# Kernel optimization log

Hardware: AMD Instinct MI355X
Metric: run time of the kernel (lower is better)

## Reference

```python
import jax, jax.numpy as jnp
import numpy as np

N_NODES, N_EDGES, DIM, N_GRAPHS = 200000, 400000, 256, 2048


def _mlp_params(key, dim):
    # MLP([dim, dim//2, dim//4, 1]) -> 3 Linear layers
    k1, k2, k3 = jax.random.split(key, 3)
    def lin(k, fi, fo):
        s = 1.0 / np.sqrt(fi)
        kw, kb = jax.random.split(k)
        W = jax.random.uniform(kw, (fi, fo), jnp.float32, -s, s)
        b = jax.random.uniform(kb, (fo,), jnp.float32, -s, s)
        return W, b
    W1, b1 = lin(k1, dim, dim // 2)
    W2, b2 = lin(k2, dim // 2, dim // 4)
    W3, b3 = lin(k3, dim // 4, 1)
    return W1, b1, W2, b2, W3, b3


def setup_inputs() -> dict:
    key = jax.random.key(0)
    kn, ke, kin, kie, kpn, kpe = jax.random.split(key, 6)
    emb_nodes = jax.random.normal(kn, (N_NODES, DIM), jnp.float32)
    emb_edges = jax.random.normal(ke, (N_EDGES, DIM), jnp.float32)
    node_index = jnp.sort(jax.random.randint(kin, (N_NODES,), 0, N_GRAPHS, jnp.int32))
    edge_index = jnp.sort(jax.random.randint(kie, (N_EDGES,), 0, N_GRAPHS, jnp.int32))
    Wn1, bn1, Wn2, bn2, Wn3, bn3 = _mlp_params(kpn, DIM)
    We1, be1, We2, be2, We3, be3 = _mlp_params(kpe, DIM)
    return {
        "emb_nodes": emb_nodes, "emb_edges": emb_edges,
        "node_index": node_index, "edge_index": edge_index,
        "Wn1": Wn1, "bn1": bn1, "Wn2": Wn2, "bn2": bn2, "Wn3": Wn3, "bn3": bn3,
        "We1": We1, "be1": be1, "We2": We2, "be2": be2, "We3": We3, "be3": be3,
        "num_graphs": N_GRAPHS,
    }


def _gated_att_pool(src, index, W1, b1, W2, b2, W3, b3, num_segments):
    # att MLP: dim -> dim/2 -> dim/4 -> 1 (ReLU between hidden layers)
    h = jax.nn.relu(src @ W1 + b1)
    h = jax.nn.relu(h @ W2 + b2)
    logits = (h @ W3 + b3).reshape(-1)  # [N]
    # scatter_softmax over segments (numerically stable)
    m = jax.ops.segment_max(logits, index, num_segments=num_segments)
    e = jnp.exp(logits - m[index])
    s = jax.ops.segment_sum(e, index, num_segments=num_segments)
    att = (e / s[index])[:, None]  # [N,1]
    # weighted scatter_add -> [num_segments, dim]
    return jax.ops.segment_sum(att * src, index, num_segments=num_segments)


def reference(emb_nodes, emb_edges, node_index, edge_index,
              Wn1, bn1, Wn2, bn2, Wn3, bn3,
              We1, be1, We2, be2, We3, be3, num_graphs):
    nodes_pooled = _gated_att_pool(emb_nodes, node_index, Wn1, bn1, Wn2, bn2, Wn3, bn3, num_graphs)
    edges_pooled = _gated_att_pool(emb_edges, edge_index, We1, be1, We2, be2, We3, be3, num_graphs)
    return nodes_pooled, edges_pooled
```

## Files before the change

### kernel.cpp

```cpp
#include <hip/hip_runtime.h>

typedef unsigned short ushort_t;
typedef __attribute__((ext_vector_type(8))) short short8;
typedef __attribute__((ext_vector_type(4))) float f32x4;

__device__ __forceinline__ ushort_t f2bf(float f) {
    union { float f; unsigned int u; } c; c.f = f;
    unsigned int r = c.u + 0x7fffu + ((c.u >> 16) & 1u);
    return (ushort_t)(r >> 16);
}

__global__ __launch_bounds__(256) void build_wfrags(
    const float* __restrict__ W1, const float* __restrict__ W2,
    ushort_t* __restrict__ W1f, ushort_t* __restrict__ W2f)
{
    int tid = blockIdx.x * 256 + threadIdx.x;
    if (tid < 32768) {
        int j = tid & 7, l = (tid >> 3) & 63, fi = tid >> 9;
        int nt = fi >> 3, kt = fi & 7;
        int n = nt * 16 + (l & 15);
        int k = kt * 32 + (l >> 4) * 8 + j;
        W1f[tid] = f2bf(W1[k * 128 + n]);
    } else if (tid < 40960) {
        int u = tid - 32768;
        int j = u & 7, l = (u >> 3) & 63, fi = u >> 9;
        int nt = fi >> 2, kt = fi & 3;
        int n = nt * 16 + (l & 15);
        int k = kt * 32 + (l >> 4) * 8 + j;
        W2f[u] = f2bf(W2[k * 64 + n]);
    }
}

#define MLP_WAVES 8
#define MLP_TPW 1
#define MLP_LDS_BYTES (16384 + MLP_WAVES * 16 * 136 * 2)

__global__ __launch_bounds__(512, 4) void mlp_logits(
    const float* __restrict__ X, const ushort_t* __restrict__ W1f,
    const ushort_t* __restrict__ W2f, const float* __restrict__ b1,
    const float* __restrict__ b2, const float* __restrict__ W3,
    const float* __restrict__ b3, float* __restrict__ logits, int nsub)
{
    extern __shared__ __align__(16) char smem[];
    ushort_t* W2s    = (ushort_t*)smem;
    ushort_t* h1base = (ushort_t*)(smem + 16384);

    const int t = threadIdx.x;
    const int w = t >> 6, lane = t & 63;
    const int q = lane >> 4, c16 = lane & 15;

    {
        const f32x4* s2 = (const f32x4*)W2f; f32x4* d2 = (f32x4*)smem;
        for (int i = t; i < 1024; i += 512) d2[i] = s2[i];
    }
    __syncthreads();

    float bias1[8], bias2[4], w3v[4];
    #pragma unroll
    for (int nt = 0; nt < 8; ++nt) bias1[nt] = b1[nt * 16 + c16];
    #pragma unroll
    for (int nt = 0; nt < 4; ++nt) bias2[nt] = b2[nt * 16 + c16];
    #pragma unroll
    for (int nt = 0; nt < 4; ++nt) w3v[nt] = W3[nt * 16 + c16];
    const float b3v = b3[0];

    ushort_t* hw = h1base + w * (16 * 136);

    for (int sub = 0; sub < MLP_TPW; ++sub) {
        const int s = (blockIdx.x * MLP_WAVES + w) * MLP_TPW + sub;
        if (s >= nsub) break;
        const float* xp = X + (size_t)(s * 16 + c16) * 256 + q * 8;

        short8 av[8];
        {
            f32x4 xv[8];
            #pragma unroll
            for (int kt = 0; kt < 4; ++kt) {
                xv[2 * kt]     = *(const f32x4*)(xp + kt * 32);
                xv[2 * kt + 1] = *(const f32x4*)(xp + kt * 32 + 4);
            }
            #pragma unroll
            for (int kt = 0; kt < 4; ++kt)
                #pragma unroll
                for (int j = 0; j < 4; ++j) {
                    av[kt][j]     = (short)f2bf(xv[2 * kt][j]);
                    av[kt][4 + j] = (short)f2bf(xv[2 * kt + 1][j]);
                }
            #pragma unroll
            for (int kt = 4; kt < 8; ++kt) {
                xv[2 * (kt - 4)]     = *(const f32x4*)(xp + kt * 32);
                xv[2 * (kt - 4) + 1] = *(const f32x4*)(xp + kt * 32 + 4);
            }
            #pragma unroll
            for (int kt = 4; kt < 8; ++kt)
                #pragma unroll
                for (int j = 0; j < 4; ++j) {
                    av[kt][j]     = (short)f2bf(xv[2 * (kt - 4)][j]);
                    av[kt][4 + j] = (short)f2bf(xv[2 * (kt - 4) + 1][j]);
                }
        }

        f32x4 acc[8];
        #pragma unroll
        for (int nt = 0; nt < 8; ++nt) acc[nt] = (f32x4){0.f, 0.f, 0.f, 0.f};
        #pragma unroll
        for (int kt = 0; kt < 8; ++kt) {
            #pragma unroll
            for (int nt = 0; nt < 8; ++nt) {
                short8 bf = *(const short8*)(W1f + ((nt * 8 + kt) * 64 + lane) * 8);
                acc[nt] = __builtin_amdgcn_mfma_f32_16x16x32_bf16(av[kt], bf, acc[nt], 0, 0, 0);
            }
        }

        #pragma unroll
        for (int nt = 0; nt < 8; ++nt)
            #pragma unroll
            for (int reg = 0; reg < 4; ++reg)
                hw[(q * 4 + reg) * 136 + nt * 16 + c16] =
                    f2bf(fmaxf(acc[nt][reg] + bias1[nt], 0.f));

        f32x4 acc2[4];
        #pragma unroll
        for (int nt = 0; nt < 4; ++nt) acc2[nt] = (f32x4){0.f, 0.f, 0.f, 0.f};
        #pragma unroll
        for (int kt = 0; kt < 4; ++kt) {
            short8 a = *(const short8*)(hw + c16 * 136 + kt * 32 + q * 8);
            #pragma unroll
            for (int nt = 0; nt < 4; ++nt) {
                short8 bf = *(const short8*)(W2s + ((nt * 4 + kt) * 64 + lane) * 8);
                acc2[nt] = __builtin_amdgcn_mfma_f32_16x16x32_bf16(a, bf, acc2[nt], 0, 0, 0);
            }
        }

        float p[4];
        #pragma unroll
        for (int reg = 0; reg < 4; ++reg) {
            float v = 0.f;
            #pragma unroll
            for (int nt = 0; nt < 4; ++nt)
                v += fmaxf(acc2[nt][reg] + bias2[nt], 0.f) * w3v[nt];
            p[reg] = v;
        }
        #pragma unroll
        for (int msk = 1; msk < 16; msk <<= 1)
            #pragma unroll
            for (int reg = 0; reg < 4; ++reg)
                p[reg] += __shfl_xor(p[reg], msk);
        if (c16 == 0) {
            #pragma unroll
            for (int reg = 0; reg < 4; ++reg)
                logits[s * 16 + q * 4 + reg] = p[reg] + b3v;
        }
    }
}

__global__ __launch_bounds__(256) void pool(
    const float* __restrict__ X, const int* __restrict__ idx,
    const float* __restrict__ logits, float* __restrict__ out, int nrows)
{
    const int g = blockIdx.x;
    const int t = threadIdx.x;
    const int w = t >> 6, lane = t & 63;

    int lo = 0, hi = nrows;
    while (lo < hi) { int mid = (lo + hi) >> 1; if (idx[mid] < g) lo = mid + 1; else hi = mid; }
    const int start = lo;
    hi = nrows;
    while (lo < hi) { int mid = (lo + hi) >> 1; if (idx[mid] < g + 1) lo = mid + 1; else hi = mid; }
    const int cnt = lo - start;

    __shared__ float red[8];
    __shared__ float parts[4][256];

    const float* lg = logits + start;

    float m = -3.0e38f;
    for (int i = t; i < cnt; i += 256) m = fmaxf(m, lg[i]);
    #pragma unroll
    for (int o = 32; o; o >>= 1) m = fmaxf(m, __shfl_xor(m, o));
    if (lane == 0) red[w] = m;
    __syncthreads();
    m = fmaxf(fmaxf(red[0], red[1]), fmaxf(red[2], red[3]));

    float ssum = 0.f;
    for (int i = t; i < cnt; i += 256) ssum += __expf(lg[i] - m);
    #pragma unroll
    for (int o = 32; o; o >>= 1) ssum += __shfl_xor(ssum, o);
    if (lane == 0) red[4 + w] = ssum;
    __syncthreads();
    ssum = red[4] + red[5] + red[6] + red[7];
    const float inv = (cnt > 0) ? 1.f / ssum : 0.f;

    f32x4 acc = {0.f, 0.f, 0.f, 0.f};
    const float* xb = X + (size_t)start * 256 + lane * 4;
    int r = w;
    for (; r + 12 < cnt; r += 16) {
        float a0 = __expf(lg[r] - m);
        float a1 = __expf(lg[r + 4] - m);
        float a2 = __expf(lg[r + 8] - m);
        float a3 = __expf(lg[r + 12] - m);
        f32x4 x0 = *(const f32x4*)(xb + (size_t)(r) * 256);
        f32x4 x1 = *(const f32x4*)(xb + (size_t)(r + 4) * 256);
        f32x4 x2 = *(const f32x4*)(xb + (size_t)(r + 8) * 256);
        f32x4 x3 = *(const f32x4*)(xb + (size_t)(r + 12) * 256);
        acc += a0 * x0;
        acc += a1 * x1;
        acc += a2 * x2;
        acc += a3 * x3;
    }
    for (; r < cnt; r += 4) {
        float a = __expf(lg[r] - m);
        f32x4 xv = *(const f32x4*)(xb + (size_t)r * 256);
        acc += a * xv;
    }
    #pragma unroll
    for (int j = 0; j < 4; ++j) parts[w][lane * 4 + j] = acc[j] * inv;
    __syncthreads();
    out[(size_t)g * 256 + t] = parts[0][t] + parts[1][t] + parts[2][t] + parts[3][t];
}


extern "C" void kernel_launch(void* const* d_in, const int* in_sizes, int n_in,
                              void* d_out, int out_size, void* d_ws, size_t ws_size,
                              hipStream_t stream) {
    const float* Xn  = (const float*)d_in[0];
    const float* Xe  = (const float*)d_in[1];
    const int* idxn  = (const int*)d_in[2];
    const int* idxe  = (const int*)d_in[3];
    const float* Wn1 = (const float*)d_in[4];
    const float* bn1 = (const float*)d_in[5];
    const float* Wn2 = (const float*)d_in[6];
    const float* bn2 = (const float*)d_in[7];
    const float* Wn3 = (const float*)d_in[8];
    const float* bn3 = (const float*)d_in[9];
    const float* We1 = (const float*)d_in[10];
    const float* be1 = (const float*)d_in[11];
    const float* We2 = (const float*)d_in[12];
    const float* be2 = (const float*)d_in[13];
    const float* We3 = (const float*)d_in[14];
    const float* be3 = (const float*)d_in[15];
    float* out = (float*)d_out;

    char* ws = (char*)d_ws;
    ushort_t* W1f_n = (ushort_t*)(ws + 0);
    ushort_t* W2f_n = (ushort_t*)(ws + 65536);
    ushort_t* W1f_e = (ushort_t*)(ws + 81920);
    ushort_t* W2f_e = (ushort_t*)(ws + 147456);
    float* log_n = (float*)(ws + 163840);
    float* log_e = (float*)(ws + 963840);

    (void)hipFuncSetAttribute((const void*)mlp_logits,
                              hipFuncAttributeMaxDynamicSharedMemorySize,
                              MLP_LDS_BYTES);

    build_wfrags<<<160, 256, 0, stream>>>(Wn1, Wn2, W1f_n, W2f_n);
    build_wfrags<<<160, 256, 0, stream>>>(We1, We2, W1f_e, W2f_e);

    const int nsub_n = 200000 / 16, nsub_e = 400000 / 16;
    const int gpb = MLP_WAVES * MLP_TPW;
    mlp_logits<<<(nsub_n + gpb - 1) / gpb, 512, MLP_LDS_BYTES, stream>>>(
        Xn, W1f_n, W2f_n, bn1, bn2, Wn3, bn3, log_n, nsub_n);
    pool<<<2048, 256, 0, stream>>>(Xn, idxn, log_n, out, 200000);

    mlp_logits<<<(nsub_e + gpb - 1) / gpb, 512, MLP_LDS_BYTES, stream>>>(
        Xe, W1f_e, W2f_e, be1, be2, We3, be3, log_e, nsub_e);
    pool<<<2048, 256, 0, stream>>>(Xe, idxe, log_e, out + (size_t)2048 * 256, 400000);
}
```

Before: 852.2 us.

## Fuse attention MLP logits with per-graph softmax pooling into one kernel

Merges the MLP logit kernel and the segment-softmax pooling kernel into a single kernel with one block per graph. Each block computes the logits for its own rows, keeps them in LDS, then runs softmax and a weighted sum over the same rows, which should now be partly cache-resident. This removes the global logits round trip and two launches. In exchange, parallelism is limited to 2048 blocks with uneven segment sizes. Logits are capped at 1024 rows per graph in LDS, with no guard for larger graphs.

```diff
diff --git a/kernel.cpp b/kernel.cpp
--- a/kernel.cpp
+++ b/kernel.cpp
@@ -31,26 +31,38 @@
     }
 }
 
-#define MLP_WAVES 8
-#define MLP_TPW 1
-#define MLP_LDS_BYTES (16384 + MLP_WAVES * 16 * 136 * 2)
-
-__global__ __launch_bounds__(512, 4) void mlp_logits(
-    const float* __restrict__ X, const ushort_t* __restrict__ W1f,
-    const ushort_t* __restrict__ W2f, const float* __restrict__ b1,
-    const float* __restrict__ b2, const float* __restrict__ W3,
-    const float* __restrict__ b3, float* __restrict__ logits, int nsub)
+#define FW_WAVES 8
+#define FUSED_CAP 1024
+#define FUSED_LDS (16384 + 34816 + 4096 + 8192 + 64)
+
+__global__ __launch_bounds__(512, 4) void fused_pool(
+    const float* __restrict__ X, const int* __restrict__ idx,
+    const ushort_t* __restrict__ W1f, const ushort_t* __restrict__ W2f,
+    const float* __restrict__ b1, const float* __restrict__ b2,
+    const float* __restrict__ W3, const float* __restrict__ b3,
+    float* __restrict__ out, int nrows)
 {
     extern __shared__ __align__(16) char smem[];
-    ushort_t* W2s    = (ushort_t*)smem;
-    ushort_t* h1base = (ushort_t*)(smem + 16384);
-
+    ushort_t* W2s      = (ushort_t*)smem;
+    ushort_t* h1base   = (ushort_t*)(smem + 16384);
+    float*    logits_s = (float*)(smem + 51200);
+    float*    parts    = (float*)(smem + 55296);
+    float*    red      = (float*)(smem + 63488);
+
+    const int g = blockIdx.x;
     const int t = threadIdx.x;
     const int w = t >> 6, lane = t & 63;
     const int q = lane >> 4, c16 = lane & 15;
 
+    int lo = 0, hi = nrows;
+    while (lo < hi) { int mid = (lo + hi) >> 1; if (idx[mid] < g) lo = mid + 1; else hi = mid; }
+    const int start = lo;
+    hi = nrows;
+    while (lo < hi) { int mid = (lo + hi) >> 1; if (idx[mid] < g + 1) lo = mid + 1; else hi = mid; }
+    const int cnt = lo - start;
+
     {
-        const f32x4* s2 = (const f32x4*)W2f; f32x4* d2 = (f32x4*)smem;
+        const f32x4* s2 = (const f32x4*)W2f; f32x4* d2 = (f32x4*)W2s;
         for (int i = t; i < 1024; i += 512) d2[i] = s2[i];
     }
     __syncthreads();
@@ -66,10 +78,11 @@
 
     ushort_t* hw = h1base + w * (16 * 136);
 
-    for (int sub = 0; sub < MLP_TPW; ++sub) {
-        const int s = (blockIdx.x * MLP_WAVES + w) * MLP_TPW + sub;
-        if (s >= nsub) break;
-        const float* xp = X + (size_t)(s * 16 + c16) * 256 + q * 8;
+    const int nsub_g = (cnt + 15) >> 4;
+    for (int sg = w; sg < nsub_g; sg += FW_WAVES) {
+        int rowi = sg * 16 + c16;
+        if (rowi >= cnt) rowi = cnt - 1;
+        const float* xp = X + (size_t)(start + rowi) * 256 + q * 8;
 
         short8 av[8];
         {
@@ -148,75 +161,66 @@
                 p[reg] += __shfl_xor(p[reg], msk);
         if (c16 == 0) {
             #pragma unroll
-            for (int reg = 0; reg < 4; ++reg)
-                logits[s * 16 + q * 4 + reg] = p[reg] + b3v;
-        }
-    }
-}
-
-__global__ __launch_bounds__(256) void pool(
-    const float* __restrict__ X, const int* __restrict__ idx,
-    const float* __restrict__ logits, float* __restrict__ out, int nrows)
-{
-    const int g = blockIdx.x;
-    const int t = threadIdx.x;
-    const int w = t >> 6, lane = t & 63;
-
-    int lo = 0, hi = nrows;
-    while (lo < hi) { int mid = (lo + hi) >> 1; if (idx[mid] < g) lo = mid + 1; else hi = mid; }
-    const int start = lo;
-    hi = nrows;
-    while (lo < hi) { int mid = (lo + hi) >> 1; if (idx[mid] < g + 1) lo = mid + 1; else hi = mid; }
-    const int cnt = lo - start;
-
-    __shared__ float red[8];
-    __shared__ float parts[4][256];
-
-    const float* lg = logits + start;
+            for (int reg = 0; reg < 4; ++reg) {
+                int r = sg * 16 + q * 4 + reg;
+                if (r < cnt) logits_s[r] = p[reg] + b3v;
+            }
+        }
+    }
+    __syncthreads();
 
     float m = -3.0e38f;
-    for (int i = t; i < cnt; i += 256) m = fmaxf(m, lg[i]);
+    for (int i = t; i < cnt; i += 512) m = fmaxf(m, logits_s[i]);
     #pragma unroll
     for (int o = 32; o; o >>= 1) m = fmaxf(m, __shfl_xor(m, o));
     if (lane == 0) red[w] = m;
     __syncthreads();
-    m = fmaxf(fmaxf(red[0], red[1]), fmaxf(red[2], red[3]));
+    m = red[0];
+    #pragma unroll
+    for (int i = 1; i < 8; ++i) m = fmaxf(m, red[i]);
 
     float ssum = 0.f;
-    for (int i = t; i < cnt; i += 256) ssum += __expf(lg[i] - m);
+    for (int i = t; i < cnt; i += 512) ssum += __expf(logits_s[i] - m);
     #pragma unroll
     for (int o = 32; o; o >>= 1) ssum += __shfl_xor(ssum, o);
-    if (lane == 0) red[4 + w] = ssum;
-    __syncthreads();
-    ssum = red[4] + red[5] + red[6] + red[7];
+    if (lane == 0) red[8 + w] = ssum;
+    __syncthreads();
+    ssum = 0.f;
+    #pragma unroll
+    for (int i = 0; i < 8; ++i) ssum += red[8 + i];
     const float inv = (cnt > 0) ? 1.f / ssum : 0.f;
 
     f32x4 acc = {0.f, 0.f, 0.f, 0.f};
     const float* xb = X + (size_t)start * 256 + lane * 4;
     int r = w;
-    for (; r + 12 < cnt; r += 16) {
-        float a0 = __expf(lg[r] - m);
-        float a1 = __expf(lg[r + 4] - m);
-        float a2 = __expf(lg[r + 8] - m);
-        float a3 = __expf(lg[r + 12] - m);
+    for (; r + 24 < cnt; r += 32) {
+        float a0 = __expf(logits_s[r] - m);
+        float a1 = __expf(logits_s[r + 8] - m);
+        float a2 = __expf(logits_s[r + 16] - m);
+        float a3 = __expf(logits_s[r + 24] - m);
         f32x4 x0 = *(const f32x4*)(xb + (size_t)(r) * 256);
-        f32x4 x1 = *(const f32x4*)(xb + (size_t)(r + 4) * 256);
-        f32x4 x2 = *(const f32x4*)(xb + (size_t)(r + 8) * 256);
-        f32x4 x3 = *(const f32x4*)(xb + (size_t)(r + 12) * 256);
+        f32x4 x1 = *(const f32x4*)(xb + (size_t)(r + 8) * 256);
+        f32x4 x2 = *(const f32x4*)(xb + (size_t)(r + 16) * 256);
+        f32x4 x3 = *(const f32x4*)(xb + (size_t)(r + 24) * 256);
         acc += a0 * x0;
         acc += a1 * x1;
         acc += a2 * x2;
         acc += a3 * x3;
     }
-    for (; r < cnt; r += 4) {
-        float a = __expf(lg[r] - m);
+    for (; r < cnt; r += 8) {
+        float a = __expf(logits_s[r] - m);
         f32x4 xv = *(const f32x4*)(xb + (size_t)r * 256);
         acc += a * xv;
     }
     #pragma unroll
-    for (int j = 0; j < 4; ++j) parts[w][lane * 4 + j] = acc[j] * inv;
-    __syncthreads();
-    out[(size_t)g * 256 + t] = parts[0][t] + parts[1][t] + parts[2][t] + parts[3][t];
+    for (int j = 0; j < 4; ++j) parts[w * 256 + lane * 4 + j] = acc[j] * inv;
+    __syncthreads();
+    if (t < 256) {
+        float v = 0.f;
+        #pragma unroll
+        for (int i = 0; i < 8; ++i) v += parts[i * 256 + t];
+        out[(size_t)g * 256 + t] = v;
+    }
 }
 
 
@@ -246,23 +250,17 @@
     ushort_t* W2f_n = (ushort_t*)(ws + 65536);
     ushort_t* W1f_e = (ushort_t*)(ws + 81920);
     ushort_t* W2f_e = (ushort_t*)(ws + 147456);
-    float* log_n = (float*)(ws + 163840);
-    float* log_e = (float*)(ws + 963840);
-
-    (void)hipFuncSetAttribute((const void*)mlp_logits,
+
+    (void)hipFuncSetAttribute((const void*)fused_pool,
                               hipFuncAttributeMaxDynamicSharedMemorySize,
-                              MLP_LDS_BYTES);
+                              FUSED_LDS);
 
     build_wfrags<<<160, 256, 0, stream>>>(Wn1, Wn2, W1f_n, W2f_n);
     build_wfrags<<<160, 256, 0, stream>>>(We1, We2, W1f_e, W2f_e);
 
-    const int nsub_n = 200000 / 16, nsub_e = 400000 / 16;
-    const int gpb = MLP_WAVES * MLP_TPW;
-    mlp_logits<<<(nsub_n + gpb - 1) / gpb, 512, MLP_LDS_BYTES, stream>>>(
-        Xn, W1f_n, W2f_n, bn1, bn2, Wn3, bn3, log_n, nsub_n);
-    pool<<<2048, 256, 0, stream>>>(Xn, idxn, log_n, out, 200000);
-
-    mlp_logits<<<(nsub_e + gpb - 1) / gpb, 512, MLP_LDS_BYTES, stream>>>(
-        Xe, W1f_e, W2f_e, be1, be2, We3, be3, log_e, nsub_e);
-    pool<<<2048, 256, 0, stream>>>(Xe, idxe, log_e, out + (size_t)2048 * 256, 400000);
-}
+    fused_pool<<<2048, 512, FUSED_LDS, stream>>>(
+        Xn, idxn, W1f_n, W2f_n, bn1, bn2, Wn3, bn3, out, 200000);
+    fused_pool<<<2048, 512, FUSED_LDS, stream>>>(
+        Xe, idxe, W1f_e, W2f_e, be1, be2, We3, be3,
+        out + (size_t)2048 * 256, 400000);
+}
```

Result: slower. 1.622 ms (+90.3%).
